# Optimization experiments

Hardware: AMD Instinct MI355X
Metric: run time of the kernel (lower is better)

The kernel has to match this reference:

```python
import jax, jax.numpy as jnp
import numpy as np

H_STEP = 0.1
DT_MOMENTUM = 1.0
NUM_STEPS = 5
PAD_IDX = 0


def setup_inputs() -> dict:
    key = jax.random.key(0)
    k0, k1, k2, k3 = jax.random.split(key, 4)
    V, D, S, H, B = 32000, 512, 1024, 2048, 32
    table = jax.random.normal(k0, (V, D), jnp.float32) * 0.02
    log_masses = jnp.zeros((S,), jnp.float32)
    W1 = jax.random.normal(k1, (H, D), jnp.float32) * (1.0 / np.sqrt(D))
    b1 = jnp.zeros((H,), jnp.float32)
    W2 = jax.random.normal(k2, (1, H), jnp.float32) * (1.0 / np.sqrt(H))
    b2 = jnp.zeros((1,), jnp.float32)
    enc_input_ids = jax.random.randint(k3, (B, S), 0, V)
    return {"table": table, "log_masses": log_masses, "W1": W1, "b1": b1,
            "W2": W2, "b2": b2, "enc_input_ids": enc_input_ids}


def reference(table, log_masses, W1, b1, W2, b2, enc_input_ids):
    # padding mask derived as ids != pad_idx (code path with enc_padding_mask=None)
    mask = (enc_input_ids != PAD_IDX).astype(jnp.float32)[..., None]  # [B,S,1]
    # nn.Embedding(padding_idx=0): row 0 is zero
    row_mask = (jnp.arange(table.shape[0]) != PAD_IDX).astype(table.dtype)[:, None]
    tab = table * row_mask
    q0 = tab[enc_input_ids]                                            # [B,S,D]
    # replicate-pad one step in front -> finite-difference velocities
    prev = jnp.concatenate([q0[:, :1], q0[:, :-1]], axis=1)
    vel = (q0 - prev) / DT_MOMENTUM
    masses = jnp.exp(log_masses)[None, :, None]                        # [1,S,1]
    p0 = masses * vel * mask

    w2 = W2[0]  # [H]

    def force(q):
        # torch detaches q before the potential; grad through forces w.r.t. q is cut
        qs = jax.lax.stop_gradient(q)
        t = jnp.tanh(qs @ W1.T + b1)                                   # [B,S,H]
        # analytic grad of sum(mask * (tanh(qW1^T+b1) @ w2 + b2)) w.r.t. q
        g = ((1.0 - t * t) * w2) @ W1                                  # [B,S,D]
        return -(mask * g)

    def step(carry, _):
        q, p = carry
        f1 = force(q)
        p_half = p + 0.5 * H_STEP * f1
        q_delta = H_STEP * (p_half / masses) * mask
        q_next = q + q_delta
        f2 = force(q_next)
        p_next = (p_half + 0.5 * H_STEP * f2) * mask
        return (q_next, p_next), None

    (q, p), _ = jax.lax.scan(step, (q0, p0), None, length=NUM_STEPS)
    return (q, p)
```

## Files before the change

kernel.cpp:

```cpp
#include <hip/hip_runtime.h>

#define D_SZ 512
#define S_SZ 1024
#define H_SZ 2048
#define BS_SZ 32768
#define H_STEP 0.1f

typedef __attribute__((ext_vector_type(4))) float f32x4;
typedef __attribute__((ext_vector_type(8))) short s16x8;
typedef __attribute__((ext_vector_type(4))) unsigned short u16x4;
typedef unsigned short ushort_t;
typedef unsigned char u8;
typedef long long i64;

__device__ __forceinline__ ushort_t f2b(float f) {
    unsigned u = __float_as_uint(f);
    unsigned r = (u + 0x7FFFu + ((u >> 16) & 1u)) >> 16;
    return (ushort_t)r;
}
__device__ __forceinline__ float b2f(ushort_t b) {
    return __uint_as_float(((unsigned)b) << 16);
}

__device__ __forceinline__ void gload_lds16(const void* g, void* l) {
    __builtin_amdgcn_global_load_lds(
        (const __attribute__((address_space(1))) unsigned int*)g,
        (__attribute__((address_space(3))) unsigned int*)l, 16, 0, 0);
}

__global__ void prep_w1(const float* __restrict__ W1,
                        ushort_t* __restrict__ W1b) {
    int idx = blockIdx.x * 256 + threadIdx.x;
    W1b[idx] = f2b(W1[idx]);
}

__global__ void prep_w1t8(const float* __restrict__ W1, u8* __restrict__ W1f8) {
    __shared__ float t[64][65];
    int hb = blockIdx.x >> 3;
    int db = blockIdx.x & 7;
    int tr = threadIdx.x >> 2;
    int tc = threadIdx.x & 3;
    const float* src = W1 + (size_t)(hb * 64 + tr) * D_SZ + db * 64 + tc * 16;
    #pragma unroll
    for (int j = 0; j < 16; j += 4) {
        f32x4 v = *(const f32x4*)(src + j);
        t[tr][tc * 16 + j + 0] = v[0];
        t[tr][tc * 16 + j + 1] = v[1];
        t[tr][tc * 16 + j + 2] = v[2];
        t[tr][tc * 16 + j + 3] = v[3];
    }
    __syncthreads();
    u8* dst = W1f8 + (size_t)(db * 64 + tr) * H_SZ + hb * 64 + tc * 16;
    #pragma unroll
    for (int j = 0; j < 16; j += 4) {
        int r = 0;
        r = __builtin_amdgcn_cvt_pk_fp8_f32(t[tc * 16 + j + 0][tr] * 8.0f,
                                            t[tc * 16 + j + 1][tr] * 8.0f, r, false);
        r = __builtin_amdgcn_cvt_pk_fp8_f32(t[tc * 16 + j + 2][tr] * 8.0f,
                                            t[tc * 16 + j + 3][tr] * 8.0f, r, true);
        *(int*)(dst + j) = r;
    }
}

__global__ void prep_mass(const float* __restrict__ logm,
                          float* __restrict__ inv_mass,
                          float* __restrict__ mass) {
    int s = blockIdx.x * 256 + threadIdx.x;
    if (s < S_SZ) {
        float lm = logm[s];
        mass[s] = expf(lm);
        inv_mass[s] = expf(-lm);
    }
}

__global__ void embed_kernel(const float* __restrict__ table,
                             const int* __restrict__ ids,
                             const float* __restrict__ mass,
                             float* __restrict__ p,
                             ushort_t* __restrict__ qb) {
    int i = blockIdx.x;
    int t = threadIdx.x;
    int s = i & (S_SZ - 1);
    int id = ids[i];
    int idp = (s == 0) ? id : ids[i - 1];
    float mk = (id != 0) ? 1.f : 0.f;
    float ms = mass[s];
    int d0 = t * 4;

    f32x4 cur = {0.f, 0.f, 0.f, 0.f};
    f32x4 prv = {0.f, 0.f, 0.f, 0.f};
    if (id != 0)  cur = *(const f32x4*)(table + (size_t)id  * D_SZ + d0);
    if (idp != 0) prv = *(const f32x4*)(table + (size_t)idp * D_SZ + d0);

    size_t off = (size_t)i * D_SZ + d0;
    u16x4 cb;
    cb[0] = f2b(cur[0]); cb[1] = f2b(cur[1]); cb[2] = f2b(cur[2]); cb[3] = f2b(cur[3]);
    *(u16x4*)(qb + off) = cb;

    f32x4 pv;
    pv[0] = ms * (cur[0] - prv[0]) * mk;
    pv[1] = ms * (cur[1] - prv[1]) * mk;
    pv[2] = ms * (cur[2] - prv[2]) * mk;
    pv[3] = ms * (cur[3] - prv[3]) * mk;
    *(f32x4*)(p + off) = pv;
}

__global__ __launch_bounds__(512, 2) void gemm_f1(
        const ushort_t* __restrict__ A,
        const ushort_t* __restrict__ B,
        const float* __restrict__ b1,
        const float* __restrict__ W2,
        u8* __restrict__ U) {
    constexpr int KLEN = 512;
    constexpr int NT = KLEN / 32;
    __shared__ __align__(16) ushort_t lA[3][256 * 32];
    __shared__ __align__(16) ushort_t lB[3][256 * 32];

    const int tid = threadIdx.x;
    const int lane = tid & 63, wid = tid >> 6;
    const int wm = wid >> 2, wn = wid & 3;
    const int lr = lane & 15, lk = lane >> 4;

    int wgid = ((int)blockIdx.x & 7) * 128 + ((int)blockIdx.x >> 3);
    int bxA = wgid & 7;
    int by  = wgid >> 3;
    const long a0 = (long)bxA * 256;
    const long b0 = (long)by * 256;

    const int r1  = tid >> 2;
    const int kc  = tid & 3;
    const int kcs = kc ^ ((r1 >> 1) & 3);
    const ushort_t* gA1 = A + (a0 + r1) * (long)KLEN + kcs * 8;
    const ushort_t* gA2 = gA1 + (long)128 * KLEN;
    const ushort_t* gB1 = B + (b0 + r1) * (long)KLEN + kcs * 8;
    const ushort_t* gB2 = gB1 + (long)128 * KLEN;
    const int ld1 = tid * 8;
    const int ld2 = (tid + 512) * 8;

#define STAGE_A(t) { int _b = (t) % 3;                         \
    gload_lds16(gA1 + (long)(t) * 32, &lA[_b][ld1]);           \
    gload_lds16(gA2 + (long)(t) * 32, &lA[_b][ld2]); }
#define STAGE_B(t) { int _b = (t) % 3;                         \
    gload_lds16(gB1 + (long)(t) * 32, &lB[_b][ld1]);           \
    gload_lds16(gB2 + (long)(t) * 32, &lB[_b][ld2]); }

    f32x4 acc[8][4];
    #pragma unroll
    for (int m = 0; m < 8; ++m)
        #pragma unroll
        for (int n = 0; n < 4; ++n)
            acc[m][n] = (f32x4){0.f, 0.f, 0.f, 0.f};

    const int lks8 = (lk ^ ((lr >> 1) & 3)) * 8;
    const int roA = (wm * 128 + lr) * 32 + lks8;
    const int roB = (wn * 64 + lr) * 32 + lks8;

    STAGE_A(0); STAGE_B(0);
    STAGE_A(1); STAGE_B(1);

    for (int t = 0; t < NT; ++t) {
        const int buf = t % 3;
        const ushort_t* bA = &lA[buf][0];
        const ushort_t* bB = &lB[buf][0];
        asm volatile("s_waitcnt vmcnt(4)" ::: "memory");
        __builtin_amdgcn_s_barrier();

        s16x8 av[4], bv[4];
        #pragma unroll
        for (int m = 0; m < 4; ++m) av[m] = *(const s16x8*)&bA[roA + m * 512];
        #pragma unroll
        for (int n = 0; n < 4; ++n) bv[n] = *(const s16x8*)&bB[roB + n * 512];
        if (t + 2 < NT) STAGE_A(t + 2);
        __builtin_amdgcn_s_setprio(1);
        #pragma unroll
        for (int m = 0; m < 4; ++m)
            #pragma unroll
            for (int n = 0; n < 4; ++n)
                acc[m][n] = __builtin_amdgcn_mfma_f32_16x16x32_bf16(av[m], bv[n], acc[m][n], 0, 0, 0);
        __builtin_amdgcn_s_setprio(0);
        __builtin_amdgcn_s_barrier();

        s16x8 av2[4];
        #pragma unroll
        for (int m = 0; m < 4; ++m) av2[m] = *(const s16x8*)&bA[roA + (m + 4) * 512];
        if (t + 2 < NT) STAGE_B(t + 2);
        __builtin_amdgcn_s_setprio(1);
        #pragma unroll
        for (int m = 0; m < 4; ++m)
            #pragma unroll
            for (int n = 0; n < 4; ++n)
                acc[m + 4][n] = __builtin_amdgcn_mfma_f32_16x16x32_bf16(av2[m], bv[n], acc[m + 4][n], 0, 0, 0);
        __builtin_amdgcn_s_setprio(0);
    }
#undef STAGE_A
#undef STAGE_B

    #pragma unroll
    for (int m = 0; m < 8; ++m) {
        long h0 = a0 + wm * 128 + m * 16 + lk * 4;
        f32x4 b1v = *(const f32x4*)(b1 + h0);
        f32x4 w2v = *(const f32x4*)(W2 + h0);
        #pragma unroll
        for (int n = 0; n < 4; ++n) {
            long i = b0 + wn * 64 + n * 16 + lr;
            float v[4];
            #pragma unroll
            for (int j = 0; j < 4; ++j) {
                float uu = acc[m][n][j] + b1v[j];
                float e = __expf(-2.0f * fabsf(uu));
                float rc = 1.0f / (1.0f + e);
                v[j] = 64.0f * e * rc * rc * w2v[j];
            }
            int pk = 0;
            pk = __builtin_amdgcn_cvt_pk_fp8_f32(v[0], v[1], pk, false);
            pk = __builtin_amdgcn_cvt_pk_fp8_f32(v[2], v[3], pk, true);
            *(int*)(U + i * H_SZ + h0) = pk;
        }
    }
}

__global__ __launch_bounds__(512, 2) void gemm_f2(
        const u8* __restrict__ W1f8,
        const u8* __restrict__ Uf8,
        const int* __restrict__ ids,
        const float* __restrict__ inv_mass,
        float* __restrict__ qf,
        float* __restrict__ p,
        ushort_t* __restrict__ qb,
        float coef, int do_q, int wq) {
    __shared__ __align__(16) u8 lA[2][256 * 64];
    __shared__ __align__(16) u8 lB[2][128 * 64];

    const int tid = threadIdx.x;
    const int lane = tid & 63, wid = tid >> 6;
    const int wd = wid >> 1, wi = wid & 1;
    const int lr = lane & 15, lk = lane >> 4;

    int wgid = ((int)blockIdx.x & 7) * 64 + ((int)blockIdx.x >> 3);
    const int  dh = wgid & 1;
    const long a0 = (long)dh * 256;
    const long b0 = (long)(wgid >> 1) * 128;

    const int r0  = tid >> 2;
    const int kc  = tid & 3;
    const int kcs = kc ^ ((r0 >> 1) & 3);
    const u8* gA = W1f8 + (a0 + r0) * (long)H_SZ + kcs * 16;
    const u8* gB = Uf8 + (b0 + r0) * (long)H_SZ + kcs * 16;

#define STG(t) { int _b = (t) & 1; \
    gload_lds16(gA + (long)(t) * 64,               &lA[_b][tid * 16]); \
    gload_lds16(gA + 128L * H_SZ + (long)(t) * 64, &lA[_b][(tid + 512) * 16]); \
    gload_lds16(gB + (long)(t) * 64,               &lB[_b][tid * 16]); }

    f32x4 acc[4][4];
    #pragma unroll
    for (int m = 0; m < 4; ++m)
        #pragma unroll
        for (int n = 0; n < 4; ++n)
            acc[m][n] = (f32x4){0.f, 0.f, 0.f, 0.f};

    const int key = (lr >> 1) & 3;

    STG(0);
    const int NT = H_SZ / 64;
    for (int t = 0; t < NT; ++t) {
        if (t + 1 < NT) {
            STG(t + 1);
            asm volatile("s_waitcnt vmcnt(3)" ::: "memory");
        } else {
            asm volatile("s_waitcnt vmcnt(0)" ::: "memory");
        }
        __builtin_amdgcn_s_barrier();

        const u8* bA = &lA[t & 1][0];
        const u8* bB = &lB[t & 1][0];
        #pragma unroll
        for (int x = 0; x < 2; ++x) {
            const int so = (((x * 2 + (lk >> 1)) ^ key) * 16) + (lk & 1) * 8;
            i64 a[4], b[4];
            #pragma unroll
            for (int m = 0; m < 4; ++m)
                a[m] = *(const i64*)&bA[(wd * 64 + m * 16 + lr) * 64 + so];
            #pragma unroll
            for (int n = 0; n < 4; ++n)
                b[n] = *(const i64*)&bB[(wi * 64 + n * 16 + lr) * 64 + so];
            asm volatile("s_waitcnt lgkmcnt(0)" ::: "memory");
            __builtin_amdgcn_sched_barrier(0);
            __builtin_amdgcn_s_setprio(1);
            #pragma unroll
            for (int m = 0; m < 4; ++m)
                #pragma unroll
                for (int n = 0; n < 4; ++n)
                    acc[m][n] = __builtin_amdgcn_mfma_f32_16x16x32_fp8_fp8(a[m], b[n], acc[m][n], 0, 0, 0);
            __builtin_amdgcn_s_setprio(0);
        }
        __builtin_amdgcn_s_barrier();
    }
#undef STG

    const float cs = coef * (1.0f / 128.0f);
    #pragma unroll
    for (int n = 0; n < 4; ++n) {
        long i = b0 + wi * 64 + n * 16 + lr;
        int id = ids[i];
        float cm = (id != 0) ? cs : 0.f;
        float hm = (id != 0) ? H_STEP : 0.f;
        float im = inv_mass[(int)(i & (S_SZ - 1))];
        #pragma unroll
        for (int m = 0; m < 4; ++m) {
            long d0 = a0 + wd * 64 + m * 16 + lk * 4;
            size_t off = (size_t)i * D_SZ + d0;
            f32x4 pv = *(const f32x4*)(p + off);
            #pragma unroll
            for (int j = 0; j < 4; ++j)
                pv[j] -= cm * acc[m][n][j];
            *(f32x4*)(p + off) = pv;
            if (do_q) {
                u16x4 qo = *(const u16x4*)(qb + off);
                f32x4 qv;
                u16x4 qn;
                #pragma unroll
                for (int j = 0; j < 4; ++j) {
                    qv[j] = b2f(qo[j]) + hm * pv[j] * im;
                    qn[j] = f2b(qv[j]);
                }
                *(u16x4*)(qb + off) = qn;
                if (wq) *(f32x4*)(qf + off) = qv;
            }
        }
    }
}

extern "C" void kernel_launch(void* const* d_in, const int* in_sizes, int n_in,
                              void* d_out, int out_size, void* d_ws, size_t ws_size,
                              hipStream_t stream) {
    const float* table = (const float*)d_in[0];
    const float* logm  = (const float*)d_in[1];
    const float* W1    = (const float*)d_in[2];
    const float* b1    = (const float*)d_in[3];
    const float* W2    = (const float*)d_in[4];
    const int*   ids   = (const int*)d_in[6];

    float* qf = (float*)d_out;
    float* p  = qf + (size_t)BS_SZ * D_SZ;

    char* ws = (char*)d_ws;
    size_t o = 0;
    ushort_t* qb  = (ushort_t*)(ws + o); o += (size_t)BS_SZ * D_SZ * 2;
    u8* Uf8       = (u8*)(ws + o);       o += (size_t)BS_SZ * H_SZ;
    ushort_t* W1b = (ushort_t*)(ws + o); o += (size_t)H_SZ * D_SZ * 2;
    u8* W1f8      = (u8*)(ws + o);       o += (size_t)D_SZ * H_SZ;
    float* inv_mass = (float*)(ws + o);  o += S_SZ * 4;
    float* mass     = (float*)(ws + o);  o += S_SZ * 4;

    prep_w1<<<(H_SZ * D_SZ) / 256, 256, 0, stream>>>(W1, W1b);
    prep_w1t8<<<256, 256, 0, stream>>>(W1, W1f8);
    prep_mass<<<(S_SZ + 255) / 256, 256, 0, stream>>>(logm, inv_mass, mass);
    embed_kernel<<<BS_SZ, 128, 0, stream>>>(table, ids, mass, p, qb);

    for (int j = 0; j < 6; ++j) {
        gemm_f1<<<1024, 512, 0, stream>>>(W1b, qb, b1, W2, Uf8);
        float coef = (j == 0 || j == 5) ? 0.05f : 0.1f;
        gemm_f2<<<512, 512, 0, stream>>>(
            W1f8, Uf8, ids, inv_mass, qf, p, qb, coef, (j < 5) ? 1 : 0, (j == 4) ? 1 : 0);
    }
}
```

Measured before the change: 1.127 ms.

## Split gemm_f1 256x256 tile across 16 waves with single-phase K loop

The gemm_f1 workgroup grows from 8 to 16 waves. Each wave now owns a 64x64 sub-tile (4x4 accumulators) instead of 128x64, which halves accumulator registers per wave, and each thread issues one A and one B global-to-LDS load per stage. The K loop drops the two half-phase MFMA split with interleaved staging. It now reads fragments, waits for LDS, runs 16 MFMAs, then issues the next stage after the barrier. This aims to hide latency through more waves, but it doubles LDS fragment reads per MFMA, adds more barrier participants, and leaves less overlap between loads and compute within a wave.

```diff
diff --git a/kernel.cpp b/kernel.cpp
--- a/kernel.cpp
+++ b/kernel.cpp
@@ -105,7 +105,7 @@
     *(f32x4*)(p + off) = pv;
 }
 
-__global__ __launch_bounds__(512, 2) void gemm_f1(
+__global__ __launch_bounds__(1024, 4) void gemm_f1(
         const ushort_t* __restrict__ A,
         const ushort_t* __restrict__ B,
         const float* __restrict__ b1,
@@ -118,7 +118,7 @@
 
     const int tid = threadIdx.x;
     const int lane = tid & 63, wid = tid >> 6;
-    const int wm = wid >> 2, wn = wid & 3;
+    const int wg = wid >> 2, wn = wid & 3;
     const int lr = lane & 15, lk = lane >> 4;
 
     int wgid = ((int)blockIdx.x & 7) * 128 + ((int)blockIdx.x >> 3);
@@ -127,42 +127,36 @@
     const long a0 = (long)bxA * 256;
     const long b0 = (long)by * 256;
 
-    const int r1  = tid >> 2;
+    const int r0  = tid >> 2;
     const int kc  = tid & 3;
-    const int kcs = kc ^ ((r1 >> 1) & 3);
-    const ushort_t* gA1 = A + (a0 + r1) * (long)KLEN + kcs * 8;
-    const ushort_t* gA2 = gA1 + (long)128 * KLEN;
-    const ushort_t* gB1 = B + (b0 + r1) * (long)KLEN + kcs * 8;
-    const ushort_t* gB2 = gB1 + (long)128 * KLEN;
-    const int ld1 = tid * 8;
-    const int ld2 = (tid + 512) * 8;
-
-#define STAGE_A(t) { int _b = (t) % 3;                         \
-    gload_lds16(gA1 + (long)(t) * 32, &lA[_b][ld1]);           \
-    gload_lds16(gA2 + (long)(t) * 32, &lA[_b][ld2]); }
-#define STAGE_B(t) { int _b = (t) % 3;                         \
-    gload_lds16(gB1 + (long)(t) * 32, &lB[_b][ld1]);           \
-    gload_lds16(gB2 + (long)(t) * 32, &lB[_b][ld2]); }
-
-    f32x4 acc[8][4];
-    #pragma unroll
-    for (int m = 0; m < 8; ++m)
+    const int kcs = kc ^ ((r0 >> 1) & 3);
+    const ushort_t* gA = A + (a0 + r0) * (long)KLEN + kcs * 8;
+    const ushort_t* gB = B + (b0 + r0) * (long)KLEN + kcs * 8;
+
+#define STAGE(t) { int _b = (t) % 3;                          \
+    gload_lds16(gA + (long)(t) * 32, &lA[_b][tid * 8]);       \
+    gload_lds16(gB + (long)(t) * 32, &lB[_b][tid * 8]); }
+
+    f32x4 acc[4][4];
+    #pragma unroll
+    for (int m = 0; m < 4; ++m)
         #pragma unroll
         for (int n = 0; n < 4; ++n)
             acc[m][n] = (f32x4){0.f, 0.f, 0.f, 0.f};
 
     const int lks8 = (lk ^ ((lr >> 1) & 3)) * 8;
-    const int roA = (wm * 128 + lr) * 32 + lks8;
+    const int roA = (wg * 64 + lr) * 32 + lks8;
     const int roB = (wn * 64 + lr) * 32 + lks8;
 
-    STAGE_A(0); STAGE_B(0);
-    STAGE_A(1); STAGE_B(1);
+    STAGE(0);
+    STAGE(1);
 
     for (int t = 0; t < NT; ++t) {
         const int buf = t % 3;
         const ushort_t* bA = &lA[buf][0];
         const ushort_t* bB = &lB[buf][0];
-        asm volatile("s_waitcnt vmcnt(4)" ::: "memory");
+        if (t < NT - 1) asm volatile("s_waitcnt vmcnt(2)" ::: "memory");
+        else           asm volatile("s_waitcnt vmcnt(0)" ::: "memory");
         __builtin_amdgcn_s_barrier();
 
         s16x8 av[4], bv[4];
@@ -170,7 +164,8 @@
         for (int m = 0; m < 4; ++m) av[m] = *(const s16x8*)&bA[roA + m * 512];
         #pragma unroll
         for (int n = 0; n < 4; ++n) bv[n] = *(const s16x8*)&bB[roB + n * 512];
-        if (t + 2 < NT) STAGE_A(t + 2);
+        asm volatile("s_waitcnt lgkmcnt(0)" ::: "memory");
+        __builtin_amdgcn_sched_barrier(0);
         __builtin_amdgcn_s_setprio(1);
         #pragma unroll
         for (int m = 0; m < 4; ++m)
@@ -179,25 +174,13 @@
                 acc[m][n] = __builtin_amdgcn_mfma_f32_16x16x32_bf16(av[m], bv[n], acc[m][n], 0, 0, 0);
         __builtin_amdgcn_s_setprio(0);
         __builtin_amdgcn_s_barrier();
-
-        s16x8 av2[4];
-        #pragma unroll
-        for (int m = 0; m < 4; ++m) av2[m] = *(const s16x8*)&bA[roA + (m + 4) * 512];
-        if (t + 2 < NT) STAGE_B(t + 2);
-        __builtin_amdgcn_s_setprio(1);
-        #pragma unroll
-        for (int m = 0; m < 4; ++m)
-            #pragma unroll
-            for (int n = 0; n < 4; ++n)
-                acc[m + 4][n] = __builtin_amdgcn_mfma_f32_16x16x32_bf16(av2[m], bv[n], acc[m + 4][n], 0, 0, 0);
-        __builtin_amdgcn_s_setprio(0);
-    }
-#undef STAGE_A
-#undef STAGE_B
-
-    #pragma unroll
-    for (int m = 0; m < 8; ++m) {
-        long h0 = a0 + wm * 128 + m * 16 + lk * 4;
+        if (t + 2 < NT) STAGE(t + 2);
+    }
+#undef STAGE
+
+    #pragma unroll
+    for (int m = 0; m < 4; ++m) {
+        long h0 = a0 + wg * 64 + m * 16 + lk * 4;
         f32x4 b1v = *(const f32x4*)(b1 + h0);
         f32x4 w2v = *(const f32x4*)(W2 + h0);
         #pragma unroll
@@ -359,7 +342,7 @@
     embed_kernel<<<BS_SZ, 128, 0, stream>>>(table, ids, mass, p, qb);
 
     for (int j = 0; j < 6; ++j) {
-        gemm_f1<<<1024, 512, 0, stream>>>(W1b, qb, b1, W2, Uf8);
+        gemm_f1<<<1024, 1024, 0, stream>>>(W1b, qb, b1, W2, Uf8);
         float coef = (j == 0 || j == 5) ? 0.05f : 0.1f;
         gemm_f2<<<512, 512, 0, stream>>>(
             W1f8, Uf8, ids, inv_mass, qf, p, qb, coef, (j < 5) ? 1 : 0, (j == 4) ? 1 : 0);
```

New measurement: 1.109 ms. No clear change (-1.6%).
